# Kernel optimization log

Measured on AMD Instinct MI355X. Metric: run time of the kernel, lower is better.

Reference implementation:

```python
import jax, jax.numpy as jnp
import numpy as np

B, L, D_MODEL, H = 2, 2048, 1024, 16
HD = D_MODEL // H  # head dim = 64


def setup_inputs() -> dict:
    key = jax.random.key(0)
    ks = jax.random.split(key, 11)
    s = 1.0 / np.sqrt(D_MODEL)
    inp = {
        "Q": jax.random.normal(ks[0], (B, L, D_MODEL), jnp.float32),
        "K": jax.random.normal(ks[1], (B, L, D_MODEL), jnp.float32),
        "V": jax.random.normal(ks[2], (B, L, D_MODEL), jnp.float32),
        "Wq": jax.random.normal(ks[3], (D_MODEL, D_MODEL), jnp.float32) * s,
        "bq": jnp.zeros((D_MODEL,), jnp.float32),
        "Wk": jax.random.normal(ks[4], (D_MODEL, D_MODEL), jnp.float32) * s,
        "bk": jnp.zeros((D_MODEL,), jnp.float32),
        "Wv": jax.random.normal(ks[5], (D_MODEL, D_MODEL), jnp.float32) * s,
        "bv": jnp.zeros((D_MODEL,), jnp.float32),
        "Wo": jax.random.normal(ks[6], (D_MODEL, D_MODEL), jnp.float32) * s,
        "bo": jnp.zeros((D_MODEL,), jnp.float32),
    }
    return inp


def _split_heads(x):
    # [B, L, H*D] -> [B, H, L, D]
    return x.reshape(B, L, H, HD).transpose(0, 2, 1, 3)


def reference(Q, K, V, Wq, bq, Wk, bk, Wv, bv, Wo, bo):
    q = _split_heads(Q @ Wq.T + bq)
    k = _split_heads(K @ Wk.T + bk)
    v = _split_heads(V @ Wv.T + bv)
    scale = 1.0 / jnp.sqrt(jnp.asarray(HD, q.dtype))
    # full [B, H, L, L] score matrix, as in the original bmm->softmax->bmm
    scores = jnp.einsum("bhqd,bhkd->bhqk", q, k) * scale
    attn = jax.nn.softmax(scores, axis=-1)
    o = jnp.einsum("bhqk,bhkd->bhqd", attn, v)
    o = o.transpose(0, 2, 1, 3).reshape(B, L, D_MODEL)  # concat heads
    return o @ Wo.T + bo
```

## Files before the change

kernel.cpp:

```cpp
#include <hip/hip_runtime.h>
#include <math.h>
#include <stdint.h>

typedef __bf16 bf16_t;
typedef __attribute__((ext_vector_type(2))) __bf16 bf16x2;
typedef __attribute__((ext_vector_type(8))) __bf16 bf16x8;
typedef __attribute__((ext_vector_type(4))) float f32x4;
typedef __attribute__((ext_vector_type(16))) float f32x16;
typedef __attribute__((address_space(1))) unsigned int gu32;
typedef __attribute__((address_space(3))) unsigned int lu32;

#define MFMA16(a, b, c) __builtin_amdgcn_mfma_f32_16x16x32_bf16((a), (b), (c), 0, 0, 0)
#define MFMA32(a, b, c) __builtin_amdgcn_mfma_f32_32x32x16_bf16((a), (b), (c), 0, 0, 0)

__device__ __forceinline__ void gll16(const void* g, void* l) {
    __builtin_amdgcn_global_load_lds((const gu32*)(uintptr_t)g,
                                     (lu32*)(uintptr_t)l, 16, 0, 0);
}

__device__ __forceinline__ bf16x8 ld_frag68(const bf16_t* p) {
    union { bf16x8 v; uint2 u[2]; } r;
    r.u[0] = *(const uint2*)p;
    r.u[1] = *(const uint2*)(p + 4);
    return r.v;
}

__global__ __launch_bounds__(256) void convert_all(
    const float* __restrict__ Q, const float* __restrict__ K, const float* __restrict__ V,
    const float* __restrict__ Wq, const float* __restrict__ Wk, const float* __restrict__ Wv,
    const float* __restrict__ Wo, bf16_t* __restrict__ dst) {
    size_t e0 = (size_t)blockIdx.x * 2048;
    const float* src; size_t off;
    if (e0 < 4194304)       { src = Q;  off = e0; }
    else if (e0 < 8388608)  { src = K;  off = e0 - 4194304; }
    else if (e0 < 12582912) { src = V;  off = e0 - 8388608; }
    else if (e0 < 13631488) { src = Wq; off = e0 - 12582912; }
    else if (e0 < 14680064) { src = Wk; off = e0 - 13631488; }
    else if (e0 < 15728640) { src = Wv; off = e0 - 14680064; }
    else                    { src = Wo; off = e0 - 15728640; }
#pragma unroll
    for (int p = 0; p < 2; ++p) {
        int t = p * 1024 + threadIdx.x * 4;
        float4 v = *(const float4*)(src + off + t);
        union { ushort4 u; bf16_t h[4]; } pk;
        pk.h[0] = (bf16_t)v.x; pk.h[1] = (bf16_t)v.y;
        pk.h[2] = (bf16_t)v.z; pk.h[3] = (bf16_t)v.w;
        *(ushort4*)(dst + e0 + t) = pk.u;
    }
}

__global__ __launch_bounds__(256) void qkv_gemm(
    const bf16_t* __restrict__ Qb, const bf16_t* __restrict__ Kb, const bf16_t* __restrict__ Vb,
    const bf16_t* __restrict__ Wqb, const bf16_t* __restrict__ Wkb, const bf16_t* __restrict__ Wvb,
    const float* __restrict__ bq, const float* __restrict__ bk, const float* __restrict__ bv,
    bf16_t* __restrict__ qo, bf16_t* __restrict__ ko, bf16_t* __restrict__ vT) {
    constexpr int Kdim = 1024, N = 1024;
    __shared__ __attribute__((aligned(16))) bf16_t smem[4 * 128 * 64];

    const int tid = threadIdx.x, wave = tid >> 6, lane = tid & 63;
    const int z = blockIdx.z;
    const bf16_t* A = (z == 0) ? Qb : (z == 1) ? Kb : Vb;
    const bf16_t* W = (z == 0) ? Wqb : (z == 1) ? Wkb : Wvb;
    const float* bias = (z == 0) ? bq : (z == 1) ? bk : bv;
    const int bm = blockIdx.x * 128, bn = blockIdx.y * 128;
    const int l16 = lane & 15, quad = lane >> 4;
    const int wm = (wave >> 1) * 64, wn = (wave & 1) * 64;
    const int grow = lane >> 3;
    const int gcol = (((lane & 7) ^ grow)) * 8;
    const int rsw = l16 & 7;

    f32x4 acc[4][4] = {};

    auto stage = [&](int k0, bf16_t* As, bf16_t* Bs) {
#pragma unroll
        for (int j = 0; j < 4; ++j) {
            int chunk = wave * 4 + j;
            int row = chunk * 8 + grow;
            gll16(A + (size_t)(bm + row) * Kdim + k0 + gcol, As + chunk * 512);
            gll16(W + (size_t)(bn + row) * Kdim + k0 + gcol, Bs + chunk * 512);
        }
    };
    auto compute = [&](const bf16_t* As, const bf16_t* Bs) {
#pragma unroll
        for (int ks = 0; ks < 64; ks += 32) {
            const int sl = ((ks >> 3) + quad);
            const int so = (sl ^ rsw) * 8;
            bf16x8 af[4], bf[4];
#pragma unroll
            for (int i = 0; i < 4; ++i)
                af[i] = *(const bf16x8*)&As[(wm + i * 16 + l16) * 64 + so];
#pragma unroll
            for (int i = 0; i < 4; ++i)
                bf[i] = *(const bf16x8*)&Bs[(wn + i * 16 + l16) * 64 + so];
#pragma unroll
            for (int i = 0; i < 4; ++i)
#pragma unroll
                for (int j = 0; j < 4; ++j)
                    acc[i][j] = MFMA16(af[i], bf[j], acc[i][j]);
        }
    };

    stage(0, smem, smem + 8192);
    asm volatile("s_waitcnt vmcnt(0)" ::: "memory");
    __builtin_amdgcn_s_barrier();
    int cur = 0;
    for (int t = 0; t < 15; ++t) {
        bf16_t* nb = smem + (cur ^ 1) * 16384;
        stage((t + 1) * 64, nb, nb + 8192);
        bf16_t* cb = smem + cur * 16384;
        compute(cb, cb + 8192);
        asm volatile("s_waitcnt vmcnt(0)" ::: "memory");
        __builtin_amdgcn_s_barrier();
        cur ^= 1;
    }
    {
        bf16_t* cb = smem + cur * 16384;
        compute(cb, cb + 8192);
    }

    if (z < 2) {
        bf16_t* outp = (z == 0) ? qo : ko;
        const float sc = (z == 0) ? 0.18033688011112042f : 1.0f;
        constexpr int RST = 132;
#pragma unroll
        for (int p = 0; p < 2; ++p) {
            __syncthreads();
            if ((wave >> 1) == p) {
#pragma unroll
                for (int mi = 0; mi < 4; ++mi)
#pragma unroll
                    for (int nj = 0; nj < 4; ++nj) {
                        int col = wn + nj * 16 + l16;
                        float bv_ = bias[bn + col];
#pragma unroll
                        for (int r = 0; r < 4; ++r) {
                            int rp = mi * 16 + quad * 4 + r;
                            smem[rp * RST + col] = (bf16_t)((acc[mi][nj][r] + bv_) * sc);
                        }
                    }
            }
            __syncthreads();
            int rp = tid >> 2;
            int cb2 = (tid & 3) * 32;
            int row = bm + p * 64 + rp;
#pragma unroll
            for (int j = 0; j < 4; ++j) {
                uint2 lo = *(const uint2*)&smem[rp * RST + cb2 + j * 8];
                uint2 hi = *(const uint2*)&smem[rp * RST + cb2 + j * 8 + 4];
                *(uint4*)&outp[(size_t)row * N + bn + cb2 + j * 8] =
                    make_uint4(lo.x, lo.y, hi.x, hi.y);
            }
        }
    } else {
#pragma unroll
        for (int mi = 0; mi < 4; ++mi)
#pragma unroll
            for (int nj = 0; nj < 4; ++nj) {
                int col = bn + wn + nj * 16 + l16;
                int h = col >> 6, d = col & 63;
                float bv_ = bias[col];
                int row0 = bm + wm + mi * 16 + quad * 4;
                int bb = row0 >> 11, l = row0 & 2047;
                int lb = (l & ~12) | ((l & 4) << 1) | ((l & 8) >> 1);
                union { ushort4 u; bf16_t h4[4]; } pk;
#pragma unroll
                for (int r = 0; r < 4; ++r) pk.h4[r] = (bf16_t)(acc[mi][nj][r] + bv_);
                *(ushort4*)&vT[(((size_t)bb * 16 + h) * 64 + d) * 2048 + lb] = pk.u;
            }
    }
}

__global__ __launch_bounds__(256) void out_gemm(const bf16_t* __restrict__ A,
                                                const bf16_t* __restrict__ W,
                                                const float* __restrict__ bias,
                                                float* __restrict__ out) {
    constexpr int Kdim = 1024, N = 1024;
    __shared__ __attribute__((aligned(16))) bf16_t smem[2 * 12288];
    const int tid = threadIdx.x, wave = tid >> 6, lane = tid & 63;
    const int bm = blockIdx.x * 64, bn = blockIdx.y * 128;
    const int l16 = lane & 15, quad = lane >> 4;
    const int wm = (wave >> 1) * 32, wn = (wave & 1) * 64;
    const int grow = lane >> 3;
    const int gcol = (((lane & 7) ^ grow)) * 8;
    const int rsw = l16 & 7;
    f32x4 acc[2][4] = {};

    auto stage = [&](int k0, bf16_t* As, bf16_t* Bs) {
#pragma unroll
        for (int j = 0; j < 2; ++j) {
            int chunk = wave * 2 + j;
            int row = chunk * 8 + grow;
            gll16(A + (size_t)(bm + row) * Kdim + k0 + gcol, As + chunk * 512);
        }
#pragma unroll
        for (int j = 0; j < 4; ++j) {
            int chunk = wave * 4 + j;
            int row = chunk * 8 + grow;
            gll16(W + (size_t)(bn + row) * Kdim + k0 + gcol, Bs + chunk * 512);
        }
    };
    auto compute = [&](const bf16_t* As, const bf16_t* Bs) {
#pragma unroll
        for (int ks = 0; ks < 64; ks += 32) {
            const int so0 = ((((ks >> 3) + quad)) ^ rsw) * 8;
            bf16x8 af[2], bf[4];
#pragma unroll
            for (int i = 0; i < 2; ++i)
                af[i] = *(const bf16x8*)&As[(wm + i * 16 + l16) * 64 + so0];
#pragma unroll
            for (int i = 0; i < 4; ++i)
                bf[i] = *(const bf16x8*)&Bs[(wn + i * 16 + l16) * 64 + so0];
#pragma unroll
            for (int i = 0; i < 2; ++i)
#pragma unroll
                for (int j = 0; j < 4; ++j)
                    acc[i][j] = MFMA16(af[i], bf[j], acc[i][j]);
        }
    };

    stage(0, smem, smem + 4096);
    asm volatile("s_waitcnt vmcnt(0)" ::: "memory");
    __builtin_amdgcn_s_barrier();
    int cur = 0;
    for (int t = 0; t < 15; ++t) {
        bf16_t* nb = smem + (cur ^ 1) * 12288;
        stage((t + 1) * 64, nb, nb + 4096);
        bf16_t* cb = smem + cur * 12288;
        compute(cb, cb + 4096);
        asm volatile("s_waitcnt vmcnt(0)" ::: "memory");
        __builtin_amdgcn_s_barrier();
        cur ^= 1;
    }
    {
        bf16_t* cb = smem + cur * 12288;
        compute(cb, cb + 4096);
    }

#pragma unroll
    for (int mi = 0; mi < 2; ++mi)
#pragma unroll
        for (int nj = 0; nj < 4; ++nj) {
            int col = bn + wn + nj * 16 + l16;
            float bv_ = bias[col];
#pragma unroll
            for (int r = 0; r < 4; ++r) {
                int row = bm + wm + mi * 16 + quad * 4 + r;
                out[(size_t)row * N + col] = acc[mi][nj][r] + bv_;
            }
        }
}

__global__ __launch_bounds__(256, 4) void attn6(const bf16_t* __restrict__ qo,
                                                const bf16_t* __restrict__ ko,
                                                const bf16_t* __restrict__ vT,
                                                bf16_t* __restrict__ Op,
                                                float* __restrict__ lpp) {
    constexpr int L = 2048, D = 1024, ST = 68;
    __shared__ __attribute__((aligned(16))) bf16_t smem[2 * 64 * ST];
    bf16_t* ksm = smem;
    bf16_t* vsm = smem + 64 * ST;

    const int tid = threadIdx.x, wave = tid >> 6, lane = tid & 63;
    const int l31 = lane & 31, hi = lane >> 5;
    const int b = blockIdx.x >> 4, h = blockIdx.x & 15;
    const int q0 = blockIdx.y * 128;
    const int split = blockIdx.z;
    bf16_t* Opart = Op + (size_t)split * 4194304;
    float* lpart = lpp + split * 65536;

    const int rloc = tid >> 2, cg = tid & 3;
    const bf16_t* kbase = ko + ((size_t)b * L + rloc) * D + h * 64 + cg * 16;
    const bf16_t* vbase = vT + (((size_t)b * 16 + h) * 64 + rloc) * L + cg * 16;

    bf16x8 qf[4];
    {
        const bf16_t* qptr = qo + ((size_t)b * L + q0 + wave * 32 + l31) * D + h * 64 + hi * 8;
#pragma unroll
        for (int ks = 0; ks < 4; ++ks) qf[ks] = *(const bf16x8*)(qptr + ks * 16);
    }

    f32x16 o0{}, o1{};
    float lpl = 0.f;

    const int kt0 = split * 16, kt1 = kt0 + 16;
    for (int kt = kt0; kt < kt1; ++kt) {
        const size_t koff = (size_t)(kt * 64) * D;
        const int voff = kt * 64;
        uint4 ka = *(const uint4*)(kbase + koff);
        uint4 kc = *(const uint4*)(kbase + koff + 8);
        uint4 va = *(const uint4*)(vbase + voff);
        uint4 vc = *(const uint4*)(vbase + voff + 8);
        __syncthreads();
        {
            bf16_t* kd = &ksm[rloc * ST + cg * 16];
            bf16_t* vd = &vsm[rloc * ST + cg * 16];
            *(uint2*)(kd + 0)  = make_uint2(ka.x, ka.y);
            *(uint2*)(kd + 4)  = make_uint2(ka.z, ka.w);
            *(uint2*)(kd + 8)  = make_uint2(kc.x, kc.y);
            *(uint2*)(kd + 12) = make_uint2(kc.z, kc.w);
            *(uint2*)(vd + 0)  = make_uint2(va.x, va.y);
            *(uint2*)(vd + 4)  = make_uint2(va.z, va.w);
            *(uint2*)(vd + 8)  = make_uint2(vc.x, vc.y);
            *(uint2*)(vd + 12) = make_uint2(vc.z, vc.w);
        }
        __syncthreads();

        f32x16 s0{}, s1{};
#pragma unroll
        for (int ks = 0; ks < 4; ++ks) {
            bf16x8 k0 = ld_frag68(&ksm[l31 * ST + ks * 16 + hi * 8]);
            bf16x8 k1 = ld_frag68(&ksm[(32 + l31) * ST + ks * 16 + hi * 8]);
            s0 = MFMA32(k0, qf[ks], s0);
            s1 = MFMA32(k1, qf[ks], s1);
        }

#pragma unroll
        for (int t = 0; t < 4; ++t) {
            union { bf16x8 v; bf16_t e[8]; } pf;
#pragma unroll
            for (int j = 0; j < 8; ++j) {
                float sv = (t < 2) ? s0[(t & 1) * 8 + j] : s1[(t & 1) * 8 + j];
                float p = __builtin_amdgcn_exp2f(sv);
                lpl += p;
                pf.e[j] = (bf16_t)p;
            }
            bf16x8 v0 = ld_frag68(&vsm[l31 * ST + t * 16 + hi * 8]);
            bf16x8 v1 = ld_frag68(&vsm[(32 + l31) * ST + t * 16 + hi * 8]);
            o0 = MFMA32(v0, pf.v, o0);
            o1 = MFMA32(v1, pf.v, o1);
        }
    }

    lpl += __shfl_xor(lpl, 32, 64);
    if (hi == 0)
        lpart[((size_t)b * 16 + h) * 2048 + q0 + wave * 32 + l31] = lpl;

    __syncthreads();
    bf16_t* ew = smem + wave * (32 * ST);
#pragma unroll
    for (int r = 0; r < 16; r += 2) {
        int d = (r & 3) + 8 * (r >> 2) + 4 * hi;
        *(bf16x2*)&ew[l31 * ST + d] = bf16x2{(bf16_t)o0[r], (bf16_t)o0[r + 1]};
        *(bf16x2*)&ew[l31 * ST + 32 + d] = bf16x2{(bf16_t)o1[r], (bf16_t)o1[r + 1]};
    }
#pragma unroll
    for (int p = 0; p < 4; ++p) {
        int rr = p * 8 + (lane >> 3);
        int cc = (lane & 7) * 8;
        uint2 lo = *(const uint2*)&ew[rr * ST + cc];
        uint2 hi2 = *(const uint2*)&ew[rr * ST + cc + 4];
        *(uint4*)&Opart[((size_t)b * L + q0 + wave * 32 + rr) * D + h * 64 + cc] =
            make_uint4(lo.x, lo.y, hi2.x, hi2.y);
    }
}

__global__ __launch_bounds__(256) void combine(const bf16_t* __restrict__ Op,
                                               const float* __restrict__ lpp,
                                               bf16_t* __restrict__ Ob) {
    const size_t c = (size_t)blockIdx.x * 256 + threadIdx.x;
    const int bl = (int)(c >> 7);
    const int h = ((int)c >> 3) & 15;
    const int bb = bl >> 11, l = bl & 2047;
    const int li = (bb * 16 + h) * 2048 + l;
    const float inv = 1.f / (lpp[li] + lpp[65536 + li]);
    union { uint4 u; bf16_t h8[8]; } a, b, o;
    a.u = *(const uint4*)(Op + c * 8);
    b.u = *(const uint4*)(Op + 4194304 + c * 8);
#pragma unroll
    for (int i = 0; i < 8; ++i)
        o.h8[i] = (bf16_t)(((float)a.h8[i] + (float)b.h8[i]) * inv);
    *(uint4*)(Ob + c * 8) = o.u;
}

extern "C" void kernel_launch(void* const* d_in, const int* in_sizes, int n_in,
                              void* d_out, int out_size, void* d_ws, size_t ws_size,
                              hipStream_t stream) {
    const float* Q  = (const float*)d_in[0];
    const float* Kx = (const float*)d_in[1];
    const float* V  = (const float*)d_in[2];
    const float* Wq = (const float*)d_in[3];
    const float* bq = (const float*)d_in[4];
    const float* Wk = (const float*)d_in[5];
    const float* bk = (const float*)d_in[6];
    const float* Wv = (const float*)d_in[7];
    const float* bv = (const float*)d_in[8];
    const float* Wo = (const float*)d_in[9];
    const float* bo = (const float*)d_in[10];

    bf16_t* ws0 = (bf16_t*)d_ws;
    bf16_t* Qb  = ws0;
    bf16_t* Kb  = ws0 + 4194304;
    bf16_t* Vb  = ws0 + 8388608;
    bf16_t* Wqb = ws0 + 12582912;
    bf16_t* Wkb = ws0 + 13631488;
    bf16_t* Wvb = ws0 + 14680064;
    bf16_t* Wob = ws0 + 15728640;
    bf16_t* vT  = ws0 + 16777216;
    bf16_t* Op  = Qb;
    bf16_t* Obf = Vb;
    float*  lpp = (float*)Wqb;
    bf16_t* qo = (bf16_t*)d_out;
    bf16_t* ko = qo + 4194304;

    convert_all<<<8192, 256, 0, stream>>>(Q, Kx, V, Wq, Wk, Wv, Wo, ws0);
    qkv_gemm<<<dim3(32, 8, 3), 256, 0, stream>>>(Qb, Kb, Vb, Wqb, Wkb, Wvb,
                                                 bq, bk, bv, qo, ko, vT);
    attn6<<<dim3(32, 16, 2), 256, 0, stream>>>(qo, ko, vT, Op, lpp);
    combine<<<2048, 256, 0, stream>>>(Op, lpp, Obf);
    out_gemm<<<dim3(64, 8), 256, 0, stream>>>(Obf, Wob, bo, (float*)d_out);
}
```

Measured before the change: 220.8 us.

## Double-buffer K/V tiles in LDS with register prefetch in attention kernel

Splits shared memory into two K/V buffers. The next tile is written into the alternate buffer while the current one is consumed, and global loads are issued two tiles ahead. This cuts the per-iteration barriers from two to one and hides global load latency behind MFMA work. Wave priority is raised around the MFMA sections. LDS usage doubles, which may limit occupancy, and more registers are held live across compute.

```diff
diff --git a/kernel.cpp b/kernel.cpp
--- a/kernel.cpp
+++ b/kernel.cpp
@@ -256,9 +256,8 @@
                                                 bf16_t* __restrict__ Op,
                                                 float* __restrict__ lpp) {
     constexpr int L = 2048, D = 1024, ST = 68;
-    __shared__ __attribute__((aligned(16))) bf16_t smem[2 * 64 * ST];
-    bf16_t* ksm = smem;
-    bf16_t* vsm = smem + 64 * ST;
+    constexpr int BUF = 2 * 64 * ST;
+    __shared__ __attribute__((aligned(16))) bf16_t smem[2 * BUF];
 
     const int tid = threadIdx.x, wave = tid >> 6, lane = tid & 63;
     const int l31 = lane & 31, hi = lane >> 5;
@@ -283,29 +282,44 @@
     float lpl = 0.f;
 
     const int kt0 = split * 16, kt1 = kt0 + 16;
-    for (int kt = kt0; kt < kt1; ++kt) {
+
+    uint4 ka, kc, va, vc;
+    auto gload = [&](int kt) {
         const size_t koff = (size_t)(kt * 64) * D;
         const int voff = kt * 64;
-        uint4 ka = *(const uint4*)(kbase + koff);
-        uint4 kc = *(const uint4*)(kbase + koff + 8);
-        uint4 va = *(const uint4*)(vbase + voff);
-        uint4 vc = *(const uint4*)(vbase + voff + 8);
-        __syncthreads();
-        {
-            bf16_t* kd = &ksm[rloc * ST + cg * 16];
-            bf16_t* vd = &vsm[rloc * ST + cg * 16];
-            *(uint2*)(kd + 0)  = make_uint2(ka.x, ka.y);
-            *(uint2*)(kd + 4)  = make_uint2(ka.z, ka.w);
-            *(uint2*)(kd + 8)  = make_uint2(kc.x, kc.y);
-            *(uint2*)(kd + 12) = make_uint2(kc.z, kc.w);
-            *(uint2*)(vd + 0)  = make_uint2(va.x, va.y);
-            *(uint2*)(vd + 4)  = make_uint2(va.z, va.w);
-            *(uint2*)(vd + 8)  = make_uint2(vc.x, vc.y);
-            *(uint2*)(vd + 12) = make_uint2(vc.z, vc.w);
-        }
-        __syncthreads();
+        ka = *(const uint4*)(kbase + koff);
+        kc = *(const uint4*)(kbase + koff + 8);
+        va = *(const uint4*)(vbase + voff);
+        vc = *(const uint4*)(vbase + voff + 8);
+    };
+    auto swrite = [&](bf16_t* buf) {
+        bf16_t* kd = &buf[rloc * ST + cg * 16];
+        bf16_t* vd = &buf[64 * ST + rloc * ST + cg * 16];
+        *(uint2*)(kd + 0)  = make_uint2(ka.x, ka.y);
+        *(uint2*)(kd + 4)  = make_uint2(ka.z, ka.w);
+        *(uint2*)(kd + 8)  = make_uint2(kc.x, kc.y);
+        *(uint2*)(kd + 12) = make_uint2(kc.z, kc.w);
+        *(uint2*)(vd + 0)  = make_uint2(va.x, va.y);
+        *(uint2*)(vd + 4)  = make_uint2(va.z, va.w);
+        *(uint2*)(vd + 8)  = make_uint2(vc.x, vc.y);
+        *(uint2*)(vd + 12) = make_uint2(vc.z, vc.w);
+    };
+
+    gload(kt0);
+    swrite(smem);
+    gload(kt0 + 1 < kt1 ? kt0 + 1 : kt1 - 1);
+    asm volatile("s_waitcnt lgkmcnt(0)" ::: "memory");
+    __builtin_amdgcn_s_barrier();
+
+    int cur = 0;
+    for (int kt = kt0; kt < kt1; ++kt) {
+        swrite(smem + (cur ^ 1) * BUF);
+        gload(kt + 2 < kt1 ? kt + 2 : kt1 - 1);
+        const bf16_t* ksm = smem + cur * BUF;
+        const bf16_t* vsm = ksm + 64 * ST;
 
         f32x16 s0{}, s1{};
+        __builtin_amdgcn_s_setprio(1);
 #pragma unroll
         for (int ks = 0; ks < 4; ++ks) {
             bf16x8 k0 = ld_frag68(&ksm[l31 * ST + ks * 16 + hi * 8]);
@@ -313,6 +327,7 @@
             s0 = MFMA32(k0, qf[ks], s0);
             s1 = MFMA32(k1, qf[ks], s1);
         }
+        __builtin_amdgcn_s_setprio(0);
 
 #pragma unroll
         for (int t = 0; t < 4; ++t) {
@@ -326,9 +341,15 @@
             }
             bf16x8 v0 = ld_frag68(&vsm[l31 * ST + t * 16 + hi * 8]);
             bf16x8 v1 = ld_frag68(&vsm[(32 + l31) * ST + t * 16 + hi * 8]);
+            __builtin_amdgcn_s_setprio(1);
             o0 = MFMA32(v0, pf.v, o0);
             o1 = MFMA32(v1, pf.v, o1);
-        }
+            __builtin_amdgcn_s_setprio(0);
+        }
+
+        asm volatile("s_waitcnt lgkmcnt(0)" ::: "memory");
+        __builtin_amdgcn_s_barrier();
+        cur ^= 1;
     }
 
     lpl += __shfl_xor(lpl, 32, 64);
```

New measurement: 222.7 us. Within noise of the previous version (+0.8%).
